# Kernel optimization log

Hardware: AMD Instinct MI355X
Metric: run time of the kernel (lower is better)

## Reference

```python
import jax, jax.numpy as jnp
import numpy as np

DIM = 256
N_HEADS = 4
B, N = 2, 4096


def setup_inputs() -> dict:
    key = jax.random.key(0)
    ks = jax.random.split(key, 10)
    s = DIM ** -0.5
    return {
        "x": jax.random.normal(ks[0], (B, N, DIM), dtype=jnp.float32),
        "q_w": jax.random.normal(ks[1], (DIM, DIM), dtype=jnp.float32) * s,
        "q_b": jnp.zeros((DIM,), dtype=jnp.float32),
        "k_w": jax.random.normal(ks[2], (DIM, DIM), dtype=jnp.float32) * s,
        "k_b": jnp.zeros((DIM,), dtype=jnp.float32),
        "v_w": jax.random.normal(ks[3], (DIM, DIM), dtype=jnp.float32) * s,
        "v_b": jnp.zeros((DIM,), dtype=jnp.float32),
        "o_w": jax.random.normal(ks[4], (DIM, DIM), dtype=jnp.float32) * s,
        "o_b": jnp.zeros((DIM,), dtype=jnp.float32),
        "tau": jnp.ones((1,), dtype=jnp.float32),
    }


def reference(x, q_w, q_b, k_w, k_b, v_w, v_b, o_w, o_b, tau):
    Bsz, Nlen, C = x.shape
    H = N_HEADS
    Dh = C // H
    scale = C ** -0.5  # source uses full dim, not head_dim
    Q = (x @ q_w.T + q_b).reshape(Bsz, Nlen, H, Dh)
    K = (x @ k_w.T + k_b).reshape(Bsz, Nlen, H, Dh)
    V = (x @ v_w.T + v_b).reshape(Bsz, Nlen, H, Dh)
    attn = jnp.einsum('bnhd,bmhd->bhnm', Q, K) * scale
    # soft-threshold gate: keep only |attn| > tau, then relu
    attn = jax.nn.relu(jnp.where(jnp.abs(attn) > tau, attn, 0.0))
    attn = jax.nn.softmax(attn, axis=-1)
    out = jnp.einsum('bhnm,bmhd->bnhd', attn, V).reshape(Bsz, Nlen, C)
    return out @ o_w.T + o_b
```

## Files before the change

kernel.cpp:

```cpp
#include <hip/hip_runtime.h>

#define SEQ   4096
#define CDIM  256
#define NHEAD 4
#define DHEAD 64
#define PSTRIDE 72
#define LOG2E 1.4426950408889634f

typedef float    f32x4 __attribute__((ext_vector_type(4)));
typedef _Float16 f16x8 __attribute__((ext_vector_type(8)));
typedef _Float16 f16x4 __attribute__((ext_vector_type(4)));
typedef _Float16 f16x2 __attribute__((ext_vector_type(2)));

__device__ __forceinline__ f16x8 cvt_frag(const float* __restrict__ p) {
    float4 f0 = *(const float4*)p;
    float4 f1 = *(const float4*)(p + 4);
    f16x8 r;
    r[0]=(_Float16)f0.x; r[1]=(_Float16)f0.y; r[2]=(_Float16)f0.z; r[3]=(_Float16)f0.w;
    r[4]=(_Float16)f1.x; r[5]=(_Float16)f1.y; r[6]=(_Float16)f1.z; r[7]=(_Float16)f1.w;
    return r;
}

__device__ __forceinline__ f16x2 pkrtz(float a, float b) {
    return __builtin_bit_cast(f16x2, __builtin_amdgcn_cvt_pkrtz(a, b));
}

__global__ __launch_bounds__(256) void sta_prep(
    const float* __restrict__ qw, const float* __restrict__ kw,
    const float* __restrict__ vw, const float* __restrict__ ow,
    _Float16* __restrict__ w16)
{
    const int mat = blockIdx.y;
    const float* src = (mat == 0) ? qw : (mat == 1) ? kw : (mat == 2) ? vw : ow;
    const int i = (blockIdx.x * 256 + threadIdx.x) * 8;
    *(f16x8*)(w16 + mat * 65536 + i) = cvt_frag(src + i);
}

__global__ __launch_bounds__(256) void sta_qkv(
    const float* __restrict__ x, const _Float16* __restrict__ w16,
    const float* __restrict__ qb, const float* __restrict__ kb, const float* __restrict__ vb,
    _Float16* __restrict__ Qo, _Float16* __restrict__ Ko, _Float16* __restrict__ Vo)
{
    const int wave = threadIdx.x >> 6;
    const int lane = threadIdx.x & 63;
    const int l15  = lane & 15;
    const int quad = lane >> 4;
    const int mat  = blockIdx.y;
    const int half = blockIdx.z;
    const int row0 = blockIdx.x * 64 + wave * 16;

    const _Float16* w    = w16 + mat * 65536;
    const float*    bias = (mat == 0) ? qb : (mat == 1) ? kb : vb;

    f16x8 xf[8];
    const float* xrow = x + (row0 + l15) * CDIM + quad * 8;
    #pragma unroll
    for (int ks = 0; ks < 8; ks++) xf[ks] = cvt_frag(xrow + ks * 32);

    #pragma unroll 1
    for (int ct = 0; ct < 8; ct++) {
        const int ctg = half * 8 + ct;
        const _Float16* wr = w + (ctg * 16 + l15) * CDIM + quad * 8;
        f32x4 acc = {0.f, 0.f, 0.f, 0.f};
        if (mat < 2) {
            #pragma unroll
            for (int ks = 0; ks < 8; ks++)
                acc = __builtin_amdgcn_mfma_f32_16x16x32_f16(*(const f16x8*)(wr + ks * 32), xf[ks], acc, 0, 0, 0);
            const float4 bv = *(const float4*)(bias + ctg * 16 + quad * 4);
            const int c0 = ctg * 16 + quad * 4;
            const int h = c0 >> 6, d0 = c0 & 63;
            const int grow = row0 + l15, b = grow >> 12, n = grow & (SEQ - 1);
            const float sc = (mat == 0) ? (0.0625f * LOG2E) : 1.0f;
            f16x4 o;
            o[0] = (_Float16)((acc[0] + bv.x) * sc);
            o[1] = (_Float16)((acc[1] + bv.y) * sc);
            o[2] = (_Float16)((acc[2] + bv.z) * sc);
            o[3] = (_Float16)((acc[3] + bv.w) * sc);
            _Float16* dst = ((mat == 0) ? Qo : Ko) + (((b * NHEAD + h) * SEQ + n) * DHEAD + d0);
            *(f16x4*)dst = o;
        } else {
            #pragma unroll
            for (int ks = 0; ks < 8; ks++)
                acc = __builtin_amdgcn_mfma_f32_16x16x32_f16(xf[ks], *(const f16x8*)(wr + ks * 32), acc, 0, 0, 0);
            const int c = ctg * 16 + l15;
            const int h = c >> 6, d = c & 63;
            const float bv = bias[c];
            const int grow0 = row0 + quad * 4, b = grow0 >> 12, n0 = grow0 & (SEQ - 1);
            f16x4 o;
            #pragma unroll
            for (int r = 0; r < 4; r++) o[r] = (_Float16)(acc[r] + bv);
            *(f16x4*)(Vo + (((b * NHEAD + h) * DHEAD + d) * SEQ + n0)) = o;
        }
    }
}

__global__ __launch_bounds__(64) void sta_attn(
    const _Float16* __restrict__ Q, const _Float16* __restrict__ K, const _Float16* __restrict__ Vt,
    const float* __restrict__ taup,
    float* __restrict__ Opart, float* __restrict__ lpart)
{
    __shared__ __align__(16) _Float16 pbuf[64 * PSTRIDE];

    const int lane = threadIdx.x;
    const int l15  = lane & 15;
    const int quad = lane >> 4;
    const int qt = blockIdx.x;
    const int bh = blockIdx.y;
    const int sp = blockIdx.z;
    const float tau2 = fmaxf(taup[0], 0.0f) * LOG2E;

    const _Float16* Qb = Q  + bh * SEQ * DHEAD;
    const _Float16* Kb = K  + bh * SEQ * DHEAD;
    const _Float16* Vb = Vt + bh * DHEAD * SEQ;

    const int q0 = qt * 64;

    f16x8 qf[4][2];
    #pragma unroll
    for (int qb = 0; qb < 4; qb++)
        #pragma unroll
        for (int ks = 0; ks < 2; ks++)
            qf[qb][ks] = *(const f16x8*)(Qb + (q0 + qb * 16 + l15) * DHEAD + ks * 32 + quad * 8);

    f32x4 O[4][4];
    #pragma unroll
    for (int qb = 0; qb < 4; qb++)
        #pragma unroll
        for (int db = 0; db < 4; db++) O[qb][db] = (f32x4){0.f, 0.f, 0.f, 0.f};
    float rs[4] = {0.f, 0.f, 0.f, 0.f};

    const int kt_beg = sp * 11 - ((sp > 4) ? (sp - 4) : 0);
    const int kt_end = kt_beg + ((sp < 4) ? 11 : 10);
    #pragma unroll 1
    for (int kt = kt_beg; kt < kt_end; kt++) {
        const int kv0 = kt * 64;

        #pragma unroll
        for (int kb = 0; kb < 4; kb++) {
            const _Float16* kp = Kb + (kv0 + kb * 16 + l15) * DHEAD + quad * 8;
            f16x8 k0 = *(const f16x8*)kp;
            f16x8 k1 = *(const f16x8*)(kp + 32);
            #pragma unroll
            for (int qb = 0; qb < 4; qb++) {
                f32x4 a = {0.f, 0.f, 0.f, 0.f};
                a = __builtin_amdgcn_mfma_f32_16x16x32_f16(k0, qf[qb][0], a, 0, 0, 0);
                a = __builtin_amdgcn_mfma_f32_16x16x32_f16(k1, qf[qb][1], a, 0, 0, 0);
                float p0 = (a[0] > tau2) ? __builtin_amdgcn_exp2f(a[0]) : 1.0f;
                float p1 = (a[1] > tau2) ? __builtin_amdgcn_exp2f(a[1]) : 1.0f;
                float p2 = (a[2] > tau2) ? __builtin_amdgcn_exp2f(a[2]) : 1.0f;
                float p3 = (a[3] > tau2) ? __builtin_amdgcn_exp2f(a[3]) : 1.0f;
                rs[qb] += (p0 + p1) + (p2 + p3);
                f16x2 lo = pkrtz(p0, p1);
                f16x2 hi = pkrtz(p2, p3);
                f16x4 pk;
                pk[0] = lo[0]; pk[1] = lo[1]; pk[2] = hi[0]; pk[3] = hi[1];
                *(f16x4*)(pbuf + (qb * 16 + l15) * PSTRIDE + kb * 16 + quad * 4) = pk;
            }
        }

        #pragma unroll
        for (int ks = 0; ks < 2; ks++) {
            f16x8 pa[4];
            #pragma unroll
            for (int qb = 0; qb < 4; qb++)
                pa[qb] = *(const f16x8*)(pbuf + (qb * 16 + l15) * PSTRIDE + ks * 32 + quad * 8);
            #pragma unroll
            for (int db = 0; db < 4; db++) {
                f16x8 vf = *(const f16x8*)(Vb + (db * 16 + l15) * SEQ + kv0 + ks * 32 + quad * 8);
                #pragma unroll
                for (int qb = 0; qb < 4; qb++)
                    O[qb][db] = __builtin_amdgcn_mfma_f32_16x16x32_f16(pa[qb], vf, O[qb][db], 0, 0, 0);
            }
        }
    }

    #pragma unroll
    for (int qb = 0; qb < 4; qb++) {
        float v = rs[qb];
        v += __shfl_xor(v, 16);
        v += __shfl_xor(v, 32);
        rs[qb] = v;
    }
    float* Ob = Opart + (size_t)((sp * 8 + bh) * SEQ + q0) * DHEAD;
    #pragma unroll
    for (int qb = 0; qb < 4; qb++)
        #pragma unroll
        for (int db = 0; db < 4; db++)
            #pragma unroll
            for (int r = 0; r < 4; r++)
                Ob[(qb * 16 + quad * 4 + r) * DHEAD + db * 16 + l15] = O[qb][db][r];
    if (quad == 0) {
        #pragma unroll
        for (int qb = 0; qb < 4; qb++)
            lpart[(sp * 8 + bh) * SEQ + q0 + qb * 16 + l15] = rs[qb];
    }
}

__global__ __launch_bounds__(256) void sta_combine(
    const float* __restrict__ Opart, const float* __restrict__ lpart,
    _Float16* __restrict__ AO)
{
    const int idx = blockIdx.x * 256 + threadIdx.x;
    const int dg = idx & 15, n = (idx >> 4) & (SEQ - 1), bh = idx >> 16;
    const int d0 = dg * 4;
    float4 o = {0.f, 0.f, 0.f, 0.f};
    float l = 0.f;
    #pragma unroll
    for (int s = 0; s < 6; s++) {
        const float4 os = *(const float4*)(Opart + (size_t)((s * 8 + bh) * SEQ + n) * DHEAD + d0);
        o.x += os.x; o.y += os.y; o.z += os.z; o.w += os.w;
        l += lpart[(s * 8 + bh) * SEQ + n];
    }
    const float inv = 1.0f / l;
    const int b = bh >> 2, h = bh & 3;
    f16x4 res;
    res[0] = (_Float16)(o.x * inv); res[1] = (_Float16)(o.y * inv);
    res[2] = (_Float16)(o.z * inv); res[3] = (_Float16)(o.w * inv);
    *(f16x4*)(AO + (size_t)(b * SEQ + n) * CDIM + h * DHEAD + d0) = res;
}

__global__ __launch_bounds__(256) void sta_oproj(
    const _Float16* __restrict__ AO, const _Float16* __restrict__ w16o,
    const float* __restrict__ ob, float* __restrict__ out)
{
    const int wave = threadIdx.x >> 6;
    const int lane = threadIdx.x & 63;
    const int l15  = lane & 15;
    const int quad = lane >> 4;
    const int row0 = blockIdx.x * 64 + wave * 16;
    const int quarter = blockIdx.y;

    f16x8 af[8];
    const _Float16* arow = AO + (row0 + l15) * CDIM + quad * 8;
    #pragma unroll
    for (int ks = 0; ks < 8; ks++) af[ks] = *(const f16x8*)(arow + ks * 32);

    #pragma unroll 1
    for (int ct = 0; ct < 4; ct++) {
        const int ctg = quarter * 4 + ct;
        const _Float16* wr = w16o + (ctg * 16 + l15) * CDIM + quad * 8;
        f32x4 acc = {0.f, 0.f, 0.f, 0.f};
        #pragma unroll
        for (int ks = 0; ks < 8; ks++)
            acc = __builtin_amdgcn_mfma_f32_16x16x32_f16(*(const f16x8*)(wr + ks * 32), af[ks], acc, 0, 0, 0);
        const float4 bv = *(const float4*)(ob + ctg * 16 + quad * 4);
        const int c0 = ctg * 16 + quad * 4;
        float4 res;
        res.x = acc[0] + bv.x; res.y = acc[1] + bv.y;
        res.z = acc[2] + bv.z; res.w = acc[3] + bv.w;
        *(float4*)(out + (size_t)(row0 + l15) * CDIM + c0) = res;
    }
}

extern "C" void kernel_launch(void* const* d_in, const int* in_sizes, int n_in,
                              void* d_out, int out_size, void* d_ws, size_t ws_size,
                              hipStream_t stream) {
    const float* x   = (const float*)d_in[0];
    const float* qw  = (const float*)d_in[1];
    const float* qb  = (const float*)d_in[2];
    const float* kw  = (const float*)d_in[3];
    const float* kb  = (const float*)d_in[4];
    const float* vw  = (const float*)d_in[5];
    const float* vb  = (const float*)d_in[6];
    const float* ow  = (const float*)d_in[7];
    const float* ob  = (const float*)d_in[8];
    const float* tau = (const float*)d_in[9];

    _Float16* w16 = (_Float16*)d_ws;
    _Float16* Q   = w16 + 262144;
    _Float16* K   = Q + 2097152;
    _Float16* Vt  = K + 2097152;
    _Float16* AO  = Vt + 2097152;
    float* Opart  = (float*)(AO + 2097152);
    float* lpart  = Opart + 12582912;

    sta_prep   <<<dim3(32, 4),      256, 0, stream>>>(qw, kw, vw, ow, w16);
    sta_qkv    <<<dim3(128, 3, 2),  256, 0, stream>>>(x, w16, qb, kb, vb, Q, K, Vt);
    sta_attn   <<<dim3(64, 8, 6),    64, 0, stream>>>(Q, K, Vt, tau, Opart, lpart);
    sta_combine<<<2048,             256, 0, stream>>>(Opart, lpart, AO);
    sta_oproj  <<<dim3(128, 4),     256, 0, stream>>>(AO, w16 + 3 * 65536, ob, (float*)d_out);
}
```

Baseline: 202.0 us.

## Fuse split-KV combine into output projection and simplify attention addressing

The separate combine kernel that reduced the six split-KV partial outputs into an fp16 AO buffer is removed. The output-projection kernel now sums the partials and normalizes them itself while building its A fragments, using a new grid of 256x2 blocks of 128 threads. This drops one launch and the AO write and read round trip, but the partial sums are now re-read by both column halves. The attention kernel also hoists per-lane LDS and K base pointers, packs P stores as uint2, and makes tau wave-uniform via readfirstlane.

```diff
diff --git a/kernel.cpp b/kernel.cpp
--- a/kernel.cpp
+++ b/kernel.cpp
@@ -107,13 +107,18 @@
     const int qt = blockIdx.x;
     const int bh = blockIdx.y;
     const int sp = blockIdx.z;
-    const float tau2 = fmaxf(taup[0], 0.0f) * LOG2E;
+    const float tau2 = __builtin_bit_cast(float, __builtin_amdgcn_readfirstlane(
+        __builtin_bit_cast(int, fmaxf(taup[0], 0.0f) * LOG2E)));
 
     const _Float16* Qb = Q  + bh * SEQ * DHEAD;
     const _Float16* Kb = K  + bh * SEQ * DHEAD;
     const _Float16* Vb = Vt + bh * DHEAD * SEQ;
 
     const int q0 = qt * 64;
+
+    _Float16* __restrict__ pwb = pbuf + l15 * PSTRIDE + quad * 4;
+    const _Float16* __restrict__ prb = pbuf + l15 * PSTRIDE + quad * 8;
+    const _Float16* __restrict__ Krow = Kb + l15 * DHEAD + quad * 8;
 
     f16x8 qf[4][2];
     #pragma unroll
@@ -134,12 +139,12 @@
     #pragma unroll 1
     for (int kt = kt_beg; kt < kt_end; kt++) {
         const int kv0 = kt * 64;
+        const _Float16* Kt = Krow + kv0 * DHEAD;
 
         #pragma unroll
         for (int kb = 0; kb < 4; kb++) {
-            const _Float16* kp = Kb + (kv0 + kb * 16 + l15) * DHEAD + quad * 8;
-            f16x8 k0 = *(const f16x8*)kp;
-            f16x8 k1 = *(const f16x8*)(kp + 32);
+            f16x8 k0 = *(const f16x8*)(Kt + kb * 16 * DHEAD);
+            f16x8 k1 = *(const f16x8*)(Kt + kb * 16 * DHEAD + 32);
             #pragma unroll
             for (int qb = 0; qb < 4; qb++) {
                 f32x4 a = {0.f, 0.f, 0.f, 0.f};
@@ -150,11 +155,10 @@
                 float p2 = (a[2] > tau2) ? __builtin_amdgcn_exp2f(a[2]) : 1.0f;
                 float p3 = (a[3] > tau2) ? __builtin_amdgcn_exp2f(a[3]) : 1.0f;
                 rs[qb] += (p0 + p1) + (p2 + p3);
-                f16x2 lo = pkrtz(p0, p1);
-                f16x2 hi = pkrtz(p2, p3);
-                f16x4 pk;
-                pk[0] = lo[0]; pk[1] = lo[1]; pk[2] = hi[0]; pk[3] = hi[1];
-                *(f16x4*)(pbuf + (qb * 16 + l15) * PSTRIDE + kb * 16 + quad * 4) = pk;
+                uint2 pku;
+                pku.x = __builtin_bit_cast(unsigned int, pkrtz(p0, p1));
+                pku.y = __builtin_bit_cast(unsigned int, pkrtz(p2, p3));
+                *(uint2*)(pwb + qb * 16 * PSTRIDE + kb * 16) = pku;
             }
         }
 
@@ -163,7 +167,7 @@
             f16x8 pa[4];
             #pragma unroll
             for (int qb = 0; qb < 4; qb++)
-                pa[qb] = *(const f16x8*)(pbuf + (qb * 16 + l15) * PSTRIDE + ks * 32 + quad * 8);
+                pa[qb] = *(const f16x8*)(prb + qb * 16 * PSTRIDE + ks * 32);
             #pragma unroll
             for (int db = 0; db < 4; db++) {
                 f16x8 vf = *(const f16x8*)(Vb + (db * 16 + l15) * SEQ + kv0 + ks * 32 + quad * 8);
@@ -196,59 +200,64 @@
     }
 }
 
-__global__ __launch_bounds__(256) void sta_combine(
+__global__ __launch_bounds__(128) void sta_oproj2(
     const float* __restrict__ Opart, const float* __restrict__ lpart,
-    _Float16* __restrict__ AO)
-{
-    const int idx = blockIdx.x * 256 + threadIdx.x;
-    const int dg = idx & 15, n = (idx >> 4) & (SEQ - 1), bh = idx >> 16;
-    const int d0 = dg * 4;
-    float4 o = {0.f, 0.f, 0.f, 0.f};
-    float l = 0.f;
-    #pragma unroll
-    for (int s = 0; s < 6; s++) {
-        const float4 os = *(const float4*)(Opart + (size_t)((s * 8 + bh) * SEQ + n) * DHEAD + d0);
-        o.x += os.x; o.y += os.y; o.z += os.z; o.w += os.w;
-        l += lpart[(s * 8 + bh) * SEQ + n];
-    }
-    const float inv = 1.0f / l;
-    const int b = bh >> 2, h = bh & 3;
-    f16x4 res;
-    res[0] = (_Float16)(o.x * inv); res[1] = (_Float16)(o.y * inv);
-    res[2] = (_Float16)(o.z * inv); res[3] = (_Float16)(o.w * inv);
-    *(f16x4*)(AO + (size_t)(b * SEQ + n) * CDIM + h * DHEAD + d0) = res;
-}
-
-__global__ __launch_bounds__(256) void sta_oproj(
-    const _Float16* __restrict__ AO, const _Float16* __restrict__ w16o,
-    const float* __restrict__ ob, float* __restrict__ out)
+    const _Float16* __restrict__ w16o, const float* __restrict__ ob,
+    float* __restrict__ out)
 {
     const int wave = threadIdx.x >> 6;
     const int lane = threadIdx.x & 63;
     const int l15  = lane & 15;
     const int quad = lane >> 4;
-    const int row0 = blockIdx.x * 64 + wave * 16;
-    const int quarter = blockIdx.y;
+    const int row0 = blockIdx.x * 32 + wave * 16;
+    const int half = blockIdx.y;
+
+    const int nglob = row0 + l15;
+    const int b = nglob >> 12, n = nglob & (SEQ - 1);
 
     f16x8 af[8];
-    const _Float16* arow = AO + (row0 + l15) * CDIM + quad * 8;
-    #pragma unroll
-    for (int ks = 0; ks < 8; ks++) af[ks] = *(const f16x8*)(arow + ks * 32);
+    #pragma unroll
+    for (int h = 0; h < 4; h++) {
+        const int bhh = b * NHEAD + h;
+        float lsum = 0.f;
+        #pragma unroll
+        for (int s = 0; s < 6; s++) lsum += lpart[(s * 8 + bhh) * SEQ + n];
+        const float inv = 1.0f / lsum;
+        #pragma unroll
+        for (int dp = 0; dp < 2; dp++) {
+            const int dh0 = dp * 32 + quad * 8;
+            float a0x=0.f,a0y=0.f,a0z=0.f,a0w=0.f,a1x=0.f,a1y=0.f,a1z=0.f,a1w=0.f;
+            #pragma unroll
+            for (int s = 0; s < 6; s++) {
+                const float* p = Opart + (size_t)((s * 8 + bhh) * SEQ + n) * DHEAD + dh0;
+                const float4 t0 = *(const float4*)p;
+                const float4 t1 = *(const float4*)(p + 4);
+                a0x += t0.x; a0y += t0.y; a0z += t0.z; a0w += t0.w;
+                a1x += t1.x; a1y += t1.y; a1z += t1.z; a1w += t1.w;
+            }
+            f16x8 v;
+            v[0] = (_Float16)(a0x * inv); v[1] = (_Float16)(a0y * inv);
+            v[2] = (_Float16)(a0z * inv); v[3] = (_Float16)(a0w * inv);
+            v[4] = (_Float16)(a1x * inv); v[5] = (_Float16)(a1y * inv);
+            v[6] = (_Float16)(a1z * inv); v[7] = (_Float16)(a1w * inv);
+            af[h * 2 + dp] = v;
+        }
+    }
 
     #pragma unroll 1
-    for (int ct = 0; ct < 4; ct++) {
-        const int ctg = quarter * 4 + ct;
+    for (int ct = 0; ct < 8; ct++) {
+        const int ctg = half * 8 + ct;
         const _Float16* wr = w16o + (ctg * 16 + l15) * CDIM + quad * 8;
         f32x4 acc = {0.f, 0.f, 0.f, 0.f};
         #pragma unroll
         for (int ks = 0; ks < 8; ks++)
             acc = __builtin_amdgcn_mfma_f32_16x16x32_f16(*(const f16x8*)(wr + ks * 32), af[ks], acc, 0, 0, 0);
-        const float4 bv = *(const float4*)(ob + ctg * 16 + quad * 4);
         const int c0 = ctg * 16 + quad * 4;
+        const float4 bv = *(const float4*)(ob + c0);
         float4 res;
         res.x = acc[0] + bv.x; res.y = acc[1] + bv.y;
         res.z = acc[2] + bv.z; res.w = acc[3] + bv.w;
-        *(float4*)(out + (size_t)(row0 + l15) * CDIM + c0) = res;
+        *(float4*)(out + (size_t)nglob * CDIM + c0) = res;
     }
 }
 
@@ -270,13 +279,11 @@
     _Float16* Q   = w16 + 262144;
     _Float16* K   = Q + 2097152;
     _Float16* Vt  = K + 2097152;
-    _Float16* AO  = Vt + 2097152;
-    float* Opart  = (float*)(AO + 2097152);
+    float* Opart  = (float*)(Vt + 2097152);
     float* lpart  = Opart + 12582912;
 
-    sta_prep   <<<dim3(32, 4),      256, 0, stream>>>(qw, kw, vw, ow, w16);
-    sta_qkv    <<<dim3(128, 3, 2),  256, 0, stream>>>(x, w16, qb, kb, vb, Q, K, Vt);
-    sta_attn   <<<dim3(64, 8, 6),    64, 0, stream>>>(Q, K, Vt, tau, Opart, lpart);
-    sta_combine<<<2048,             256, 0, stream>>>(Opart, lpart, AO);
-    sta_oproj  <<<dim3(128, 4),     256, 0, stream>>>(AO, w16 + 3 * 65536, ob, (float*)d_out);
-}
+    sta_prep  <<<dim3(32, 4),      256, 0, stream>>>(qw, kw, vw, ow, w16);
+    sta_qkv   <<<dim3(128, 3, 2),  256, 0, stream>>>(x, w16, qb, kb, vb, Q, K, Vt);
+    sta_attn  <<<dim3(64, 8, 6),    64, 0, stream>>>(Q, K, Vt, tau, Opart, lpart);
+    sta_oproj2<<<dim3(256, 2),     128, 0, stream>>>(Opart, lpart, w16 + 3 * 65536, ob, (float*)d_out);
+}
```

Result: no change. 205.1 us (+1.5%).
